# Performance work log

Hardware: AMD Instinct MI355X
Metric: run time of the kernel (lower is better)

## Reference

```python
import jax, jax.numpy as jnp
import numpy as np

DIM = 1024
NUM_HEADS = 16
HEAD_DIM = DIM // NUM_HEADS
SCALE = DIM ** (-0.5)  # NOTE: original scales by full dim, not head_dim


def setup_inputs() -> dict:
    key = jax.random.key(0)
    ks = jax.random.split(key, 5)
    B, S = 2, 2048
    x = jax.random.normal(ks[0], (B, S, DIM), dtype=jnp.float32)
    w_qkv = jax.random.normal(ks[1], (DIM, 3 * DIM), dtype=jnp.float32) * (DIM ** -0.5)
    b_qkv = jax.random.normal(ks[2], (3 * DIM,), dtype=jnp.float32) * 0.02
    w_proj = jax.random.normal(ks[3], (DIM, DIM), dtype=jnp.float32) * (DIM ** -0.5)
    b_proj = jax.random.normal(ks[4], (DIM,), dtype=jnp.float32) * 0.02
    return {"x": x, "w_qkv": w_qkv, "b_qkv": b_qkv, "w_proj": w_proj, "b_proj": b_proj}


def reference(x, w_qkv, b_qkv, w_proj, b_proj):
    B, S, D = x.shape
    qkv = x @ w_qkv + b_qkv                                  # [B,S,3D]
    qkv = qkv.reshape(B, S, NUM_HEADS, 3 * HEAD_DIM).transpose(0, 2, 1, 3)  # [B,H,S,3hd]
    q, k, v = jnp.split(qkv, 3, axis=-1)                     # each [B,H,S,hd]
    attn = jnp.einsum("bhqd,bhkd->bhqk", q, k) * SCALE       # [B,H,S,S]
    attn = jax.nn.softmax(attn, axis=-1)
    out = jnp.einsum("bhqk,bhkd->bhqd", attn, v)             # [B,H,S,hd]
    out = out.transpose(0, 2, 1, 3).reshape(B, S, D)
    return out @ w_proj + b_proj
```

## Files before the change

kernel.cpp:

```cpp
#include <hip/hip_runtime.h>
#include <hip/hip_bf16.h>

#define DIM 1024
#define NH 16
#define HD 64
#define BB 2
#define SS 2048
#define MROWS (BB * SS)
#define SCALE 0.03125f
#define SC_LOG2E 0.04508422002778011f

typedef unsigned short u16;
typedef unsigned int u32;
typedef __attribute__((ext_vector_type(8))) short short8;
typedef __attribute__((ext_vector_type(4))) float f32x4;

__device__ __forceinline__ u16 f2bf(float f) {
  union { float f; u32 u; } v; v.f = f;
  return (u16)((v.u + 0x7fffu + ((v.u >> 16) & 1u)) >> 16);
}

__device__ __forceinline__ u32 pack2bf(float a, float b) {
  union { __hip_bfloat162 h; u32 u; } cv;
  cv.h = __float22bfloat162_rn(make_float2(a, b));
  return cv.u;
}

__device__ __forceinline__ void async16(const u16* g, u16* l) {
  __builtin_amdgcn_global_load_lds(
      (const __attribute__((address_space(1))) void*)(const void*)g,
      (__attribute__((address_space(3))) void*)(void*)l, 16, 0, 0);
}

__device__ __forceinline__ short8 ld8(const u16* p) { return *(const short8*)p; }

__global__ void cvt_kernel(const float* __restrict__ in, u16* __restrict__ out, int n4) {
  int i = blockIdx.x * blockDim.x + threadIdx.x;
  if (i < n4) {
    float4 v = ((const float4*)in)[i];
    u32 lo = (u32)f2bf(v.x) | ((u32)f2bf(v.y) << 16);
    u32 hi = (u32)f2bf(v.z) | ((u32)f2bf(v.w) << 16);
    ((uint2*)out)[i] = make_uint2(lo, hi);
  }
}

__global__ void tconv_kernel(const float* __restrict__ in, u16* __restrict__ out, int R, int C) {
  __shared__ u16 t[64 * 65];
  int c0 = blockIdx.x * 64, r0 = blockIdx.y * 64;
  #pragma unroll
  for (int i = 0; i < 16; i++) {
    int j = i * 256 + threadIdx.x;
    int rr = j >> 6, cc = j & 63;
    t[rr * 65 + cc] = f2bf(in[(size_t)(r0 + rr) * C + c0 + cc]);
  }
  __syncthreads();
  #pragma unroll
  for (int i = 0; i < 16; i++) {
    int j = i * 256 + threadIdx.x;
    int oc = j >> 6, orr = j & 63;
    out[(size_t)(c0 + oc) * R + r0 + orr] = t[orr * 65 + oc];
  }
}

template <int MODE>
__global__ __launch_bounds__(256, 2) void gemm_bt(
    const u16* __restrict__ A, const u16* __restrict__ Bt,
    const float* __restrict__ bias, void* __restrict__ C,
    u16* __restrict__ vT, int M, int N, int K) {
  __shared__ __align__(16) u16 As[128 * 32];
  __shared__ __align__(16) u16 Bs[128 * 32];
  const int tid = threadIdx.x;
  const int w = tid >> 6, l = tid & 63;
  const int r = l & 15, q = l >> 4;
  const int m0 = blockIdx.y * 128, n0 = blockIdx.x * 128;
  const int qm = (w & 1) * 64, qn = (w >> 1) * 64;

  const size_t aoff = (size_t)(m0 + w * 16 + (l >> 2)) * K + (size_t)(l & 3) * 8;
  const size_t boff = (size_t)(n0 + w * 16 + (l >> 2)) * K + (size_t)(l & 3) * 8;
  u16* alds = &As[(w * 64 + l) * 8];
  u16* blds = &Bs[(w * 64 + l) * 8];

  f32x4 acc[4][4] = {};
  for (int k0 = 0; k0 < K; k0 += 32) {
    async16(A + aoff + k0, alds);
    async16(A + aoff + (size_t)64 * K + k0, alds + 2048);
    async16(Bt + boff + k0, blds);
    async16(Bt + boff + (size_t)64 * K + k0, blds + 2048);
    __syncthreads();
    short8 af[4], bfr[4];
    #pragma unroll
    for (int i = 0; i < 4; i++) af[i] = ld8(&As[(qm + i * 16 + r) * 32 + q * 8]);
    #pragma unroll
    for (int j = 0; j < 4; j++) bfr[j] = ld8(&Bs[(qn + j * 16 + r) * 32 + q * 8]);
    #pragma unroll
    for (int i = 0; i < 4; i++)
      #pragma unroll
      for (int j = 0; j < 4; j++)
        acc[i][j] = __builtin_amdgcn_mfma_f32_16x16x32_bf16(af[i], bfr[j], acc[i][j], 0, 0, 0);
    __syncthreads();
  }
  #pragma unroll
  for (int i = 0; i < 4; i++) {
    int ro = m0 + qm + i * 16 + q * 4;
    #pragma unroll
    for (int j = 0; j < 4; j++) {
      int col = n0 + qn + j * 16 + r;
      float bv = bias[col];
      float v0 = acc[i][j][0] + bv, v1 = acc[i][j][1] + bv;
      float v2 = acc[i][j][2] + bv, v3 = acc[i][j][3] + bv;
      if (MODE == 1) {
        float* out = (float*)C;
        out[(size_t)(ro + 0) * N + col] = v0;
        out[(size_t)(ro + 1) * N + col] = v1;
        out[(size_t)(ro + 2) * N + col] = v2;
        out[(size_t)(ro + 3) * N + col] = v3;
      } else {
        int h = col / 192, wi = col - h * 192;
        if (wi >= 128) {
          int bb = ro >> 11, s = ro & 2047, d = wi - 128;
          uint2 pk = make_uint2(pack2bf(v0, v1), pack2bf(v2, v3));
          *(uint2*)&vT[((size_t)((bb * NH + h) * HD + d)) * SS + s] = pk;
        } else {
          u16* qk2 = (u16*)C;
          qk2[(size_t)(ro + 0) * 2048 + h * 128 + wi] = f2bf(v0);
          qk2[(size_t)(ro + 1) * 2048 + h * 128 + wi] = f2bf(v1);
          qk2[(size_t)(ro + 2) * 2048 + h * 128 + wi] = f2bf(v2);
          qk2[(size_t)(ro + 3) * 2048 + h * 128 + wi] = f2bf(v3);
        }
      }
    }
  }
}

__global__ __launch_bounds__(256, 2) void attn3_kernel(
    const u16* __restrict__ qk2, const u16* __restrict__ vT,
    u16* __restrict__ attno) {
  __shared__ __align__(16) u16 Ks[128 * 64];
  __shared__ __align__(16) u16 Vs[64 * 128];
  __shared__ __align__(16) u16 pb[4][32 * 136];
  const int tid = threadIdx.x;
  const int w = tid >> 6, l = tid & 63;
  const int r = l & 15, q = l >> 4;
  const int b = blockIdx.z, h = blockIdx.y, q0 = blockIdx.x * 128;

  const u16* qb = qk2 + (size_t)b * SS * 2048;
  const u16* kB = qb + h * 128 + 64;
  const u16* vB = vT + (size_t)((b * NH + h) * HD) * SS;
  u16* pw = &pb[w][0];

  short8 qf[2][2];
  #pragma unroll
  for (int i = 0; i < 2; i++)
    #pragma unroll
    for (int kq = 0; kq < 2; kq++)
      qf[i][kq] = ld8(qb + (size_t)(q0 + w * 32 + i * 16 + r) * 2048 + h * 128 + kq * 32 + q * 8);

  const int klrow = l >> 3;
  const int kchunk = (l & 7) ^ klrow;
  const int vlrow = l >> 4;
  const int vslot = l & 15;

  f32x4 oacc[2][4] = {};
  float lacc[2] = {0.f, 0.f};

  for (int kv0 = 0; kv0 < SS; kv0 += 128) {
    #pragma unroll
    for (int t = 0; t < 4; t++) {
      int sl = (w * 4 + t) * 8 + klrow;
      async16(kB + (size_t)(kv0 + sl) * 2048 + kchunk * 8, &Ks[(w * 4 + t) * 512 + l * 8]);
    }
    #pragma unroll
    for (int t = 0; t < 4; t++) {
      int d = (w * 4 + t) * 4 + vlrow;
      int c = vslot ^ (t * 4 + vlrow);
      async16(vB + (size_t)d * SS + kv0 + c * 8, &Vs[(w * 4 + t) * 512 + l * 8]);
    }
    __syncthreads();

    f32x4 sacc[8][2] = {};
    #pragma unroll
    for (int j = 0; j < 8; j++) {
      int sl = j * 16 + r;
      short8 a0 = ld8(&Ks[sl * 64 + ((q ^ (r & 7)) * 8)]);
      short8 a1 = ld8(&Ks[sl * 64 + (((4 + q) ^ (r & 7)) * 8)]);
      #pragma unroll
      for (int i = 0; i < 2; i++) {
        sacc[j][i] = __builtin_amdgcn_mfma_f32_16x16x32_bf16(a0, qf[i][0], sacc[j][i], 0, 0, 0);
        sacc[j][i] = __builtin_amdgcn_mfma_f32_16x16x32_bf16(a1, qf[i][1], sacc[j][i], 0, 0, 0);
      }
    }
    float rs0 = 0.f, rs1 = 0.f;
    #pragma unroll
    for (int j = 0; j < 8; j++)
      #pragma unroll
      for (int i = 0; i < 2; i++) {
        float p0 = __builtin_exp2f(sacc[j][i][0] * SC_LOG2E);
        float p1 = __builtin_exp2f(sacc[j][i][1] * SC_LOG2E);
        float p2 = __builtin_exp2f(sacc[j][i][2] * SC_LOG2E);
        float p3 = __builtin_exp2f(sacc[j][i][3] * SC_LOG2E);
        if (i == 0) rs0 += (p0 + p1) + (p2 + p3);
        else        rs1 += (p0 + p1) + (p2 + p3);
        uint2 pk = make_uint2(pack2bf(p0, p1), pack2bf(p2, p3));
        *(uint2*)&pw[(i * 16 + r) * 136 + j * 16 + q * 4] = pk;
      }
    rs0 += __shfl_xor(rs0, 16); rs0 += __shfl_xor(rs0, 32);
    rs1 += __shfl_xor(rs1, 16); rs1 += __shfl_xor(rs1, 32);
    lacc[0] += rs0;
    lacc[1] += rs1;
    #pragma unroll
    for (int ks = 0; ks < 4; ks++) {
      short8 pa0 = ld8(&pw[(size_t)r * 136 + ks * 32 + q * 8]);
      short8 pa1 = ld8(&pw[(size_t)(16 + r) * 136 + ks * 32 + q * 8]);
      #pragma unroll
      for (int dj = 0; dj < 4; dj++) {
        short8 vb = ld8(&Vs[(dj * 16 + r) * 128 + (((ks * 4 + q) ^ r) * 8)]);
        oacc[0][dj] = __builtin_amdgcn_mfma_f32_16x16x32_bf16(pa0, vb, oacc[0][dj], 0, 0, 0);
        oacc[1][dj] = __builtin_amdgcn_mfma_f32_16x16x32_bf16(pa1, vb, oacc[1][dj], 0, 0, 0);
      }
    }
    __syncthreads();
  }
  #pragma unroll
  for (int i = 0; i < 2; i++)
    #pragma unroll
    for (int e = 0; e < 4; e++) {
      float dn = __shfl(lacc[i], q * 4 + e, 16);
      float di = 1.f / dn;
      int row = q0 + w * 32 + i * 16 + q * 4 + e;
      #pragma unroll
      for (int dj = 0; dj < 4; dj++)
        attno[(size_t)(b * SS + row) * DIM + h * HD + dj * 16 + r] =
            f2bf(oacc[i][dj][e] * di);
    }
}

extern "C" void kernel_launch(void* const* d_in, const int* in_sizes, int n_in,
                              void* d_out, int out_size, void* d_ws, size_t ws_size,
                              hipStream_t stream) {
  const float* x      = (const float*)d_in[0];
  const float* w_qkv  = (const float*)d_in[1];
  const float* b_qkv  = (const float*)d_in[2];
  const float* w_proj = (const float*)d_in[3];
  const float* b_proj = (const float*)d_in[4];
  float* out = (float*)d_out;
  char* ws = (char*)d_ws;
  u16* xb     = (u16*)(ws);
  u16* wqkvT  = (u16*)(ws + ((size_t)8  << 20));
  u16* wprojT = (u16*)(ws + ((size_t)14 << 20));
  u16* qk2    = (u16*)(ws + ((size_t)16 << 20));
  u16* attno  = (u16*)(ws + ((size_t)32 << 20));
  u16* vT     = (u16*)(ws + ((size_t)40 << 20));

  cvt_kernel<<<4096, 256, 0, stream>>>(x, xb, MROWS * DIM / 4);
  tconv_kernel<<<dim3(48, 16), 256, 0, stream>>>(w_qkv, wqkvT, DIM, 3 * DIM);
  tconv_kernel<<<dim3(16, 16), 256, 0, stream>>>(w_proj, wprojT, DIM, DIM);
  gemm_bt<0><<<dim3(24, 32), 256, 0, stream>>>(xb, wqkvT, b_qkv, qk2, vT, MROWS, 3 * DIM, DIM);
  attn3_kernel<<<dim3(16, NH, BB), 256, 0, stream>>>(qk2, vT, attno);
  gemm_bt<1><<<dim3(8, 32), 256, 0, stream>>>(attno, wprojT, b_proj, out, nullptr, MROWS, DIM, DIM);
}
```

Measured before the change: 216.1 us.

## Split KV tile across two wave groups, fold softmax scale into Q, MFMA row sums

The attention kernel now runs 512 threads per block, so two groups of four waves each handle half of every 128-key tile. Their partial outputs and denominators are combined through shared memory at the end. The softmax scale times log2(e) is folded into Q in the QKV GEMM epilogue, and the raw hardware exp2 builtin is used. Row sums are computed by an MFMA against a ones vector, replacing the shuffle reductions. The aim is more waves in flight and fewer VALU ops per element, at the cost of a final cross-wave reduction and more accumulator work.

```diff
diff --git a/kernel.cpp b/kernel.cpp
--- a/kernel.cpp
+++ b/kernel.cpp
@@ -14,6 +14,12 @@
 typedef unsigned int u32;
 typedef __attribute__((ext_vector_type(8))) short short8;
 typedef __attribute__((ext_vector_type(4))) float f32x4;
+
+#if __has_builtin(__builtin_amdgcn_exp2f)
+#define EXP2(x) __builtin_amdgcn_exp2f(x)
+#else
+#define EXP2(x) __builtin_exp2f(x)
+#endif
 
 __device__ __forceinline__ u16 f2bf(float f) {
   union { float f; u32 u; } v; v.f = f;
@@ -122,116 +128,143 @@
           *(uint2*)&vT[((size_t)((bb * NH + h) * HD + d)) * SS + s] = pk;
         } else {
           u16* qk2 = (u16*)C;
-          qk2[(size_t)(ro + 0) * 2048 + h * 128 + wi] = f2bf(v0);
-          qk2[(size_t)(ro + 1) * 2048 + h * 128 + wi] = f2bf(v1);
-          qk2[(size_t)(ro + 2) * 2048 + h * 128 + wi] = f2bf(v2);
-          qk2[(size_t)(ro + 3) * 2048 + h * 128 + wi] = f2bf(v3);
+          const float sc = (wi < 64) ? SC_LOG2E : 1.0f;
+          qk2[(size_t)(ro + 0) * 2048 + h * 128 + wi] = f2bf(v0 * sc);
+          qk2[(size_t)(ro + 1) * 2048 + h * 128 + wi] = f2bf(v1 * sc);
+          qk2[(size_t)(ro + 2) * 2048 + h * 128 + wi] = f2bf(v2 * sc);
+          qk2[(size_t)(ro + 3) * 2048 + h * 128 + wi] = f2bf(v3 * sc);
         }
       }
     }
   }
 }
 
-__global__ __launch_bounds__(256, 2) void attn3_kernel(
+__global__ __launch_bounds__(512, 4) void attn4_kernel(
     const u16* __restrict__ qk2, const u16* __restrict__ vT,
     u16* __restrict__ attno) {
-  __shared__ __align__(16) u16 Ks[128 * 64];
-  __shared__ __align__(16) u16 Vs[64 * 128];
-  __shared__ __align__(16) u16 pb[4][32 * 136];
+  __shared__ __align__(16) u16 smem[34816];
+  u16* Ks = smem;
+  u16* Vs = smem + 8192;
   const int tid = threadIdx.x;
   const int w = tid >> 6, l = tid & 63;
   const int r = l & 15, q = l >> 4;
+  const int wq = w & 3, ws = w >> 2;
   const int b = blockIdx.z, h = blockIdx.y, q0 = blockIdx.x * 128;
 
   const u16* qb = qk2 + (size_t)b * SS * 2048;
   const u16* kB = qb + h * 128 + 64;
   const u16* vB = vT + (size_t)((b * NH + h) * HD) * SS;
-  u16* pw = &pb[w][0];
+  u16* pw = smem + 16384 + w * (32 * 72);
 
   short8 qf[2][2];
   #pragma unroll
   for (int i = 0; i < 2; i++)
     #pragma unroll
     for (int kq = 0; kq < 2; kq++)
-      qf[i][kq] = ld8(qb + (size_t)(q0 + w * 32 + i * 16 + r) * 2048 + h * 128 + kq * 32 + q * 8);
+      qf[i][kq] = ld8(qb + (size_t)(q0 + wq * 32 + i * 16 + r) * 2048 + h * 128 + kq * 32 + q * 8);
 
   const int klrow = l >> 3;
   const int kchunk = (l & 7) ^ klrow;
   const int vlrow = l >> 4;
   const int vslot = l & 15;
 
+  const short8 vone = {0x3F80, 0x3F80, 0x3F80, 0x3F80, 0x3F80, 0x3F80, 0x3F80, 0x3F80};
   f32x4 oacc[2][4] = {};
-  float lacc[2] = {0.f, 0.f};
+  f32x4 den[2] = {};
 
   for (int kv0 = 0; kv0 < SS; kv0 += 128) {
     #pragma unroll
-    for (int t = 0; t < 4; t++) {
-      int sl = (w * 4 + t) * 8 + klrow;
-      async16(kB + (size_t)(kv0 + sl) * 2048 + kchunk * 8, &Ks[(w * 4 + t) * 512 + l * 8]);
-    }
-    #pragma unroll
-    for (int t = 0; t < 4; t++) {
-      int d = (w * 4 + t) * 4 + vlrow;
-      int c = vslot ^ (t * 4 + vlrow);
-      async16(vB + (size_t)d * SS + kv0 + c * 8, &Vs[(w * 4 + t) * 512 + l * 8]);
-    }
-    __syncthreads();
-
-    f32x4 sacc[8][2] = {};
-    #pragma unroll
-    for (int j = 0; j < 8; j++) {
-      int sl = j * 16 + r;
-      short8 a0 = ld8(&Ks[sl * 64 + ((q ^ (r & 7)) * 8)]);
-      short8 a1 = ld8(&Ks[sl * 64 + (((4 + q) ^ (r & 7)) * 8)]);
+    for (int t = 0; t < 2; t++) {
+      int g = w * 2 + t;
+      async16(kB + (size_t)(kv0 + g * 8 + klrow) * 2048 + kchunk * 8, &Ks[g * 512 + l * 8]);
+    }
+    #pragma unroll
+    for (int t = 0; t < 2; t++) {
+      int g = w * 2 + t;
+      int d = g * 4 + vlrow;
+      int c = vslot ^ (d & 15);
+      async16(vB + (size_t)d * SS + kv0 + c * 8, &Vs[g * 512 + l * 8]);
+    }
+    __syncthreads();
+
+    f32x4 sacc[4][2] = {};
+    #pragma unroll
+    for (int j2 = 0; j2 < 4; j2++) {
+      const u16* krow = &Ks[(ws * 64 + j2 * 16 + r) * 64];
+      short8 a0 = ld8(krow + ((q ^ (r & 7)) * 8));
+      short8 a1 = ld8(krow + (((4 + q) ^ (r & 7)) * 8));
       #pragma unroll
       for (int i = 0; i < 2; i++) {
-        sacc[j][i] = __builtin_amdgcn_mfma_f32_16x16x32_bf16(a0, qf[i][0], sacc[j][i], 0, 0, 0);
-        sacc[j][i] = __builtin_amdgcn_mfma_f32_16x16x32_bf16(a1, qf[i][1], sacc[j][i], 0, 0, 0);
-      }
-    }
-    float rs0 = 0.f, rs1 = 0.f;
-    #pragma unroll
-    for (int j = 0; j < 8; j++)
+        sacc[j2][i] = __builtin_amdgcn_mfma_f32_16x16x32_bf16(a0, qf[i][0], sacc[j2][i], 0, 0, 0);
+        sacc[j2][i] = __builtin_amdgcn_mfma_f32_16x16x32_bf16(a1, qf[i][1], sacc[j2][i], 0, 0, 0);
+      }
+    }
+    #pragma unroll
+    for (int j2 = 0; j2 < 4; j2++)
       #pragma unroll
       for (int i = 0; i < 2; i++) {
-        float p0 = __builtin_exp2f(sacc[j][i][0] * SC_LOG2E);
-        float p1 = __builtin_exp2f(sacc[j][i][1] * SC_LOG2E);
-        float p2 = __builtin_exp2f(sacc[j][i][2] * SC_LOG2E);
-        float p3 = __builtin_exp2f(sacc[j][i][3] * SC_LOG2E);
-        if (i == 0) rs0 += (p0 + p1) + (p2 + p3);
-        else        rs1 += (p0 + p1) + (p2 + p3);
-        uint2 pk = make_uint2(pack2bf(p0, p1), pack2bf(p2, p3));
-        *(uint2*)&pw[(i * 16 + r) * 136 + j * 16 + q * 4] = pk;
-      }
-    rs0 += __shfl_xor(rs0, 16); rs0 += __shfl_xor(rs0, 32);
-    rs1 += __shfl_xor(rs1, 16); rs1 += __shfl_xor(rs1, 32);
-    lacc[0] += rs0;
-    lacc[1] += rs1;
-    #pragma unroll
-    for (int ks = 0; ks < 4; ks++) {
-      short8 pa0 = ld8(&pw[(size_t)r * 136 + ks * 32 + q * 8]);
-      short8 pa1 = ld8(&pw[(size_t)(16 + r) * 136 + ks * 32 + q * 8]);
+        float p0 = EXP2(sacc[j2][i][0]);
+        float p1 = EXP2(sacc[j2][i][1]);
+        float p2 = EXP2(sacc[j2][i][2]);
+        float p3 = EXP2(sacc[j2][i][3]);
+        *(uint2*)&pw[(i * 16 + r) * 72 + j2 * 16 + q * 4] =
+            make_uint2(pack2bf(p0, p1), pack2bf(p2, p3));
+      }
+    #pragma unroll
+    for (int ks = 0; ks < 2; ks++) {
+      short8 pa0 = ld8(&pw[r * 72 + ks * 32 + q * 8]);
+      short8 pa1 = ld8(&pw[(16 + r) * 72 + ks * 32 + q * 8]);
+      den[0] = __builtin_amdgcn_mfma_f32_16x16x32_bf16(pa0, vone, den[0], 0, 0, 0);
+      den[1] = __builtin_amdgcn_mfma_f32_16x16x32_bf16(pa1, vone, den[1], 0, 0, 0);
       #pragma unroll
       for (int dj = 0; dj < 4; dj++) {
-        short8 vb = ld8(&Vs[(dj * 16 + r) * 128 + (((ks * 4 + q) ^ r) * 8)]);
+        short8 vb = ld8(&Vs[(dj * 16 + r) * 128 + (((ws * 8 + ks * 4 + q) ^ r) * 8)]);
         oacc[0][dj] = __builtin_amdgcn_mfma_f32_16x16x32_bf16(pa0, vb, oacc[0][dj], 0, 0, 0);
         oacc[1][dj] = __builtin_amdgcn_mfma_f32_16x16x32_bf16(pa1, vb, oacc[1][dj], 0, 0, 0);
       }
     }
     __syncthreads();
   }
-  #pragma unroll
-  for (int i = 0; i < 2; i++)
-    #pragma unroll
-    for (int e = 0; e < 4; e++) {
-      float dn = __shfl(lacc[i], q * 4 + e, 16);
-      float di = 1.f / dn;
-      int row = q0 + w * 32 + i * 16 + q * 4 + e;
-      #pragma unroll
-      for (int dj = 0; dj < 4; dj++)
-        attno[(size_t)(b * SS + row) * DIM + h * HD + dj * 16 + r] =
-            f2bf(oacc[i][dj][e] * di);
-    }
+
+  float* part = (float*)smem;
+  float* dnf  = part + 8 * 32 * 36;
+  const int ho = 1 - ws;
+  {
+    const int wbase = (wq * 2 + ho) * 32;
+    #pragma unroll
+    for (int i = 0; i < 2; i++) {
+      if (ws == 0) {
+        *(f32x4*)&part[(wbase + r) * 36 + i * 16 + q * 4]      = oacc[i][2];
+        *(f32x4*)&part[(wbase + 16 + r) * 36 + i * 16 + q * 4] = oacc[i][3];
+      } else {
+        *(f32x4*)&part[(wbase + r) * 36 + i * 16 + q * 4]      = oacc[i][0];
+        *(f32x4*)&part[(wbase + 16 + r) * 36 + i * 16 + q * 4] = oacc[i][1];
+      }
+      if (r == 0)
+        *(f32x4*)&dnf[(ws * 4 + wq) * 32 + i * 16 + q * 4] = den[i];
+    }
+  }
+  __syncthreads();
+  {
+    const int rbase = (wq * 2 + ws) * 32;
+    #pragma unroll
+    for (int i = 0; i < 2; i++) {
+      f32x4 dt = *(f32x4*)&dnf[(ho * 4 + wq) * 32 + i * 16 + q * 4] + den[i];
+      f32x4 oa, ob;
+      if (ws == 0) { oa = oacc[i][0]; ob = oacc[i][1]; }
+      else         { oa = oacc[i][2]; ob = oacc[i][3]; }
+      oa += *(f32x4*)&part[(rbase + r) * 36 + i * 16 + q * 4];
+      ob += *(f32x4*)&part[(rbase + 16 + r) * 36 + i * 16 + q * 4];
+      #pragma unroll
+      for (int e = 0; e < 4; e++) {
+        float di = 1.f / dt[e];
+        int row = q0 + wq * 32 + i * 16 + q * 4 + e;
+        u16* o = &attno[(size_t)(b * SS + row) * DIM + h * HD + ws * 32 + r];
+        o[0]  = f2bf(oa[e] * di);
+        o[16] = f2bf(ob[e] * di);
+      }
+    }
+  }
 }
 
 extern "C" void kernel_launch(void* const* d_in, const int* in_sizes, int n_in,
@@ -255,6 +288,6 @@
   tconv_kernel<<<dim3(48, 16), 256, 0, stream>>>(w_qkv, wqkvT, DIM, 3 * DIM);
   tconv_kernel<<<dim3(16, 16), 256, 0, stream>>>(w_proj, wprojT, DIM, DIM);
   gemm_bt<0><<<dim3(24, 32), 256, 0, stream>>>(xb, wqkvT, b_qkv, qk2, vT, MROWS, 3 * DIM, DIM);
-  attn3_kernel<<<dim3(16, NH, BB), 256, 0, stream>>>(qk2, vT, attno);
+  attn4_kernel<<<dim3(16, NH, BB), 512, 0, stream>>>(qk2, vT, attno);
   gemm_bt<1><<<dim3(8, 32), 256, 0, stream>>>(attno, wprojT, b_proj, out, nullptr, MROWS, DIM, DIM);
 }
```

Result: faster. 196.3 us (-9.2%).
